# Optimization experiments

Hardware: AMD Instinct MI355X
Metric: run time of the kernel (lower is better)

The kernel has to match this reference:

```python
import jax, jax.numpy as jnp
import numpy as np

SOS = 1
H = 1024
E = 512
V = 32000


def setup_inputs() -> dict:
    key = jax.random.key(0)
    ks = jax.random.split(key, 16)
    B, T_enc, T = 32, 128, 64
    s = 1.0 / np.sqrt(H)
    inp = {
        'encoder_outputs': jax.random.normal(ks[0], (B, T_enc, H), jnp.float32),
        'encoder_hidden': jax.random.normal(ks[1], (1, B, H), jnp.float32),
        'encoder_cell': jax.random.normal(ks[2], (1, B, H), jnp.float32),
        'target_tensor': jax.random.randint(ks[3], (B, T), 0, V),
        'emb_table': jax.random.normal(ks[4], (V, E), jnp.float32) * 0.02,
        'Wa': jax.random.normal(ks[5], (H, H), jnp.float32) * s,
        'Ua': jax.random.normal(ks[6], (H, H), jnp.float32) * s,
        'Va_w': jax.random.normal(ks[7], (1, H), jnp.float32) * s,
        'Va_b': jnp.zeros((1,), jnp.float32),
        'W_ih': jax.random.normal(ks[8], (4 * H, E + H), jnp.float32) * s,
        'W_hh': jax.random.normal(ks[9], (4 * H, H), jnp.float32) * s,
        'b_ih': jnp.zeros((4 * H,), jnp.float32),
        'b_hh': jnp.zeros((4 * H,), jnp.float32),
        'fc_w': jax.random.normal(ks[10], (V, H), jnp.float32) * s,
        'fc_b': jnp.zeros((V,), jnp.float32),
    }
    return inp


def reference(encoder_outputs, encoder_hidden, encoder_cell, target_tensor,
              emb_table, Wa, Ua, Va_w, Va_b, W_ih, W_hh, b_ih, b_hh, fc_w, fc_b):
    B, T = target_tensor.shape
    # padding_idx=0: embedding row 0 is zeros
    emb_table = emb_table.at[0].set(0.0)
    enc_Ua = jnp.einsum('bth,kh->btk', encoder_outputs, Ua)  # precompute Ua(enc)
    # teacher forcing always: inputs are [SOS, target[:, :-1]], shape [T, B]
    tok_seq = jnp.concatenate([jnp.full((B, 1), SOS, target_tensor.dtype),
                               target_tensor[:, :-1]], axis=1).T

    def step(carry, tok):
        h, c = carry  # [B, H]
        emb = emb_table[tok]  # [B, E]
        # Bahdanau attention (query = last-layer hidden)
        q = h @ Wa.T  # [B, H]
        energy = jnp.tanh(q[:, None, :] + enc_Ua)  # [B, T_enc, H]
        scores = jnp.einsum('bth,h->bt', energy, Va_w[0]) + Va_b[0]
        w = jax.nn.softmax(scores, axis=1)
        context = jnp.einsum('bt,bth->bh', w, encoder_outputs)
        x = jnp.concatenate([emb, context], axis=1)  # [B, E+H]
        gates = x @ W_ih.T + b_ih + h @ W_hh.T + b_hh  # [B, 4H], order i,f,g,o
        i, f, g, o = jnp.split(gates, 4, axis=1)
        c = jax.nn.sigmoid(f) * c + jax.nn.sigmoid(i) * jnp.tanh(g)
        h = jax.nn.sigmoid(o) * jnp.tanh(c)
        logp = jax.nn.log_softmax(h @ fc_w.T + fc_b, axis=1)  # [B, V]
        return (h, c), logp

    (h, c), logps = jax.lax.scan(step, (encoder_hidden[0], encoder_cell[0]), tok_seq)
    outputs = jnp.transpose(logps, (1, 0, 2))  # [B, T, V]
    return outputs
```

## Files before the change

kernel.cpp:

```cpp
#include <hip/hip_runtime.h>
#include <math.h>

#define NB 32
#define TE 128
#define NT 64
#define HH 1024
#define EE 512
#define VV 32000
#define GG 4096
#define WQN 5120
#define NBLK 512

typedef __attribute__((ext_vector_type(8))) short bh8;
typedef __attribute__((ext_vector_type(4))) float fx4;
typedef __attribute__((ext_vector_type(4))) unsigned ux4;
typedef __attribute__((ext_vector_type(4))) float fv4;

__device__ __forceinline__ float tanh_fast(float x) {
  float e = __expf(2.f * x);
  return 1.f - 2.f / (e + 1.f);
}
__device__ __forceinline__ float sigf(float x) { return 1.f / (1.f + __expf(-x)); }
__device__ __forceinline__ ushort f2bf(float x) {
  union { float f; unsigned u; } v; v.f = x;
  unsigned r = v.u + 0x7fffu + ((v.u >> 16) & 1u);
  return (ushort)(r >> 16);
}
__device__ __forceinline__ float bf2f(ushort u) {
  return __uint_as_float(((unsigned)u) << 16);
}

__device__ __forceinline__ void st_f32(float* p, float v) {
  __hip_atomic_store(p, v, __ATOMIC_RELAXED, __HIP_MEMORY_SCOPE_AGENT);
}
__device__ __forceinline__ float ld_f32(const float* p) {
  return __hip_atomic_load(p, __ATOMIC_RELAXED, __HIP_MEMORY_SCOPE_AGENT);
}
__device__ __forceinline__ void st_u32(unsigned* p, unsigned v) {
  __hip_atomic_store(p, v, __ATOMIC_RELAXED, __HIP_MEMORY_SCOPE_AGENT);
}
__device__ __forceinline__ unsigned ld_u32(const unsigned* p) {
  return __hip_atomic_load(p, __ATOMIC_RELAXED, __HIP_MEMORY_SCOPE_AGENT);
}

__global__ void k_init(const float* __restrict__ eh, unsigned* __restrict__ h_u32) {
  int i = blockIdx.x * 256 + threadIdx.x;
  float a = eh[i * 2], b = eh[i * 2 + 1];
  h_u32[i] = (unsigned)f2bf(a) | ((unsigned)f2bf(b) << 16);
}

__global__ void k_emb(const int* __restrict__ tgt, const float* __restrict__ etab,
                      ushort* __restrict__ emb_bf) {
  int idx = blockIdx.x * 256 + threadIdx.x;
  int e = idx & (EE - 1);
  int tb = idx >> 9;
  int b = tb & (NB - 1);
  int t = tb >> 5;
  int tok = (t == 0) ? 1 : tgt[b * NT + (t - 1)];
  emb_bf[idx] = (tok == 0) ? (ushort)0 : f2bf(etab[(size_t)tok * EE + e]);
}

__global__ void k_f2b(const float* __restrict__ s, ushort* __restrict__ d, int n4) {
  int i = blockIdx.x * 256 + threadIdx.x;
  if (i >= n4) return;
  float4 v = *(const float4*)(s + (size_t)i * 4);
  *(ushort4*)(d + (size_t)i * 4) = make_ushort4(f2bf(v.x), f2bf(v.y), f2bf(v.z), f2bf(v.w));
}

__global__ void k_f2b_s(const float* __restrict__ s, int ld, int off, int w4,
                        ushort* __restrict__ d, int n) {
  int i = blockIdx.x * 256 + threadIdx.x;
  if (i >= n) return;
  int r = i / w4, c = (i - r * w4) * 4;
  float4 v = *(const float4*)(s + (size_t)r * ld + off + c);
  *(ushort4*)(d + (size_t)r * (w4 * 4) + c) = make_ushort4(f2bf(v.x), f2bf(v.y), f2bf(v.z), f2bf(v.w));
}

__device__ __forceinline__ void stage_pair(const ushort* A, int lda, const ushort* B, int ldb,
    int m0, int n0, int k0, ushort* ldsA, ushort* ldsB, int tid) {
  const int w = tid >> 6;
  const int row = tid >> 2;
  const int kq = (tid & 3) * 8;
  const ushort* ga = A + (size_t)(m0 + row) * lda + k0 + kq;
  const ushort* gb = B + (size_t)(n0 + row) * ldb + k0 + kq;
  ushort* la = ldsA + w * 512;
  ushort* lb = ldsB + w * 512;
  __builtin_amdgcn_global_load_lds((const __attribute__((address_space(1))) void*)ga,
      (__attribute__((address_space(3))) void*)la, 16, 0, 0);
  __builtin_amdgcn_global_load_lds((const __attribute__((address_space(1))) void*)(ga + (size_t)64 * lda),
      (__attribute__((address_space(3))) void*)(la + 2048), 16, 0, 0);
  __builtin_amdgcn_global_load_lds((const __attribute__((address_space(1))) void*)gb,
      (__attribute__((address_space(3))) void*)lb, 16, 0, 0);
  __builtin_amdgcn_global_load_lds((const __attribute__((address_space(1))) void*)(gb + (size_t)64 * ldb),
      (__attribute__((address_space(3))) void*)(lb + 2048), 16, 0, 0);
}

__global__ __launch_bounds__(256) void k_gemm_bf16(
    const ushort* __restrict__ A, int lda,
    const ushort* __restrict__ B, int ldb,
    const float* __restrict__ b1, const float* __restrict__ b2,
    void* __restrict__ Cv, int ldc, int K, int perm, int obf, int swz) {
  __shared__ ushort lds[2][2][4096];
  const int tid = threadIdx.x;
  const int lane = tid & 63, w = tid >> 6;
  int m0, n0;
  if (swz) {
    const int bid = blockIdx.y * gridDim.x + blockIdx.x;
    m0 = (bid & 15) * 128;
    n0 = (bid >> 4) * 128;
  } else {
    m0 = blockIdx.y * 128;
    n0 = blockIdx.x * 128;
  }
  const int wm = (w >> 1) * 64, wn = (w & 1) * 64;
  fx4 acc[4][4] = {};
  stage_pair(A, lda, B, ldb, m0, n0, 0, lds[0][0], lds[0][1], tid);
  __syncthreads();
  const int nk = K >> 5;
  const int ko = (lane >> 4) * 8;
  const int rA = wm + (lane & 15);
  const int rB = wn + (lane & 15);
  for (int ks = 0; ks < nk; ++ks) {
    const int cur = ks & 1;
    if (ks + 1 < nk)
      stage_pair(A, lda, B, ldb, m0, n0, (ks + 1) << 5, lds[cur ^ 1][0], lds[cur ^ 1][1], tid);
    bh8 af[4], bfr[4];
#pragma unroll
    for (int f = 0; f < 4; ++f) {
      af[f]  = *(const bh8*)(&lds[cur][0][(rA + f * 16) * 32 + ko]);
      bfr[f] = *(const bh8*)(&lds[cur][1][(rB + f * 16) * 32 + ko]);
    }
#pragma unroll
    for (int i = 0; i < 4; ++i)
#pragma unroll
      for (int j = 0; j < 4; ++j)
        acc[i][j] = __builtin_amdgcn_mfma_f32_16x16x32_bf16(af[i], bfr[j], acc[i][j], 0, 0, 0);
    __syncthreads();
  }
  float* Cf = (float*)Cv;
  ushort* Cb = (ushort*)Cv;
#pragma unroll
  for (int j = 0; j < 4; ++j) {
    const int col = n0 + wn + j * 16 + (lane & 15);
    const float bv = (b1 ? b1[col] : 0.f) + (b2 ? b2[col] : 0.f);
#pragma unroll
    for (int i = 0; i < 4; ++i) {
      const int mb = m0 + wm + i * 16 + (lane >> 4) * 4;
#pragma unroll
      for (int r = 0; r < 4; ++r) {
        const int m = mb + r;
        const size_t orow = perm ? ((size_t)(m & 31) * 64 + (m >> 5)) : (size_t)m;
        const float v = acc[i][j][r] + bv;
        if (obf) Cb[orow * (size_t)ldc + col] = f2bf(v);
        else     Cf[orow * (size_t)ldc + col] = v;
      }
    }
  }
}

__device__ __forceinline__ void gridbar(unsigned* flags, unsigned* genArr, unsigned epoch) {
  asm volatile("s_waitcnt vmcnt(0)" ::: "memory");
  __syncthreads();
  const int tid = threadIdx.x;
  if (tid == 0) st_u32(flags + blockIdx.x * 32, epoch);
  if (blockIdx.x == 0) {
    while (ld_u32(flags + tid * 32) < epoch) __builtin_amdgcn_s_sleep(1);
    while (ld_u32(flags + (256 + tid) * 32) < epoch) __builtin_amdgcn_s_sleep(1);
    __syncthreads();
    if (tid < 16) st_u32(genArr + tid * 32, epoch);
  } else if (tid == 0) {
    while (ld_u32(genArr + (blockIdx.x & 15) * 32) < epoch) __builtin_amdgcn_s_sleep(1);
  }
  __syncthreads();
}

__global__ __launch_bounds__(256, 1) void k_recur(
    const ushort* __restrict__ Wqh,
    const ushort* __restrict__ encU,
    const ushort* __restrict__ encW,
    const float*  __restrict__ embG,
    const float*  __restrict__ Va,
    const float*  __restrict__ ec,
    float* __restrict__ hW,
    float* __restrict__ sc,
    unsigned* __restrict__ h_u32,
    ushort* __restrict__ hall,
    unsigned* __restrict__ flags, unsigned* __restrict__ genArr) {
  const int bid = blockIdx.x;
  const int tid = threadIdx.x;
  const int lane = tid & 63, w = tid >> 6;
  __shared__ float wlds[4][32][33];
  __shared__ float red[128], wt[TE], gp[4][64];
  __shared__ float cpart[8][4][8][8];
  unsigned epoch = 0;

  const int b3 = bid >> 4, u0 = (bid & 15) * 64;
  float c_r = 0.f;
  if (tid < 64) c_r = ec[b3 * HH + u0 + tid];
  const int bb = bid >> 4, tc = bid & 15;

  for (int t = 0; t < NT; ++t) {
    if (bid < 160) {
      const int n0 = bid * 32;
      const int kb = w * 256;
      const int r15 = lane & 15, ko = (lane >> 4) * 8;
      const char* hbase0 = (const char*)h_u32 + r15 * 2048 + (size_t)(kb + ko) * 2;
      const char* hbase1 = hbase0 + 16 * 2048;
      const ushort* B0 = Wqh + (size_t)(n0 + r15) * HH + kb + ko;
      const ushort* B1 = B0 + 16 * HH;
      fx4 a00 = {}, a01 = {}, a10 = {}, a11 = {};
#pragma unroll
      for (int half = 0; half < 2; ++half) {
        union { ux4 u; bh8 b; } h0[4], h1[4];
        const char* p0 = hbase0 + half * 256;
        const char* p1 = hbase1 + half * 256;
        asm volatile(
          "global_load_dwordx4 %0, %8, off sc0 sc1\n\t"
          "global_load_dwordx4 %1, %8, off offset:64 sc0 sc1\n\t"
          "global_load_dwordx4 %2, %8, off offset:128 sc0 sc1\n\t"
          "global_load_dwordx4 %3, %8, off offset:192 sc0 sc1\n\t"
          "global_load_dwordx4 %4, %9, off sc0 sc1\n\t"
          "global_load_dwordx4 %5, %9, off offset:64 sc0 sc1\n\t"
          "global_load_dwordx4 %6, %9, off offset:128 sc0 sc1\n\t"
          "global_load_dwordx4 %7, %9, off offset:192 sc0 sc1\n\t"
          "s_waitcnt vmcnt(0)"
          : "=&v"(h0[0].u), "=&v"(h0[1].u), "=&v"(h0[2].u), "=&v"(h0[3].u),
            "=&v"(h1[0].u), "=&v"(h1[1].u), "=&v"(h1[2].u), "=&v"(h1[3].u)
          : "v"(p0), "v"(p1));
#pragma unroll
        for (int ks = 0; ks < 4; ++ks) {
          const int k = (half * 4 + ks) * 32;
          bh8 bv0 = *(const bh8*)(B0 + k);
          bh8 bv1 = *(const bh8*)(B1 + k);
          a00 = __builtin_amdgcn_mfma_f32_16x16x32_bf16(h0[ks].b, bv0, a00, 0, 0, 0);
          a01 = __builtin_amdgcn_mfma_f32_16x16x32_bf16(h0[ks].b, bv1, a01, 0, 0, 0);
          a10 = __builtin_amdgcn_mfma_f32_16x16x32_bf16(h1[ks].b, bv0, a10, 0, 0, 0);
          a11 = __builtin_amdgcn_mfma_f32_16x16x32_bf16(h1[ks].b, bv1, a11, 0, 0, 0);
        }
      }
      const int rr = (lane >> 4) * 4;
#pragma unroll
      for (int r = 0; r < 4; ++r) {
        wlds[w][rr + r][r15]           = a00[r];
        wlds[w][rr + r][r15 + 16]      = a01[r];
        wlds[w][16 + rr + r][r15]      = a10[r];
        wlds[w][16 + rr + r][r15 + 16] = a11[r];
      }
      __syncthreads();
      const int row = tid >> 3, c0 = (tid & 7) * 4;
      fv4 s4;
      s4.x = wlds[0][row][c0+0] + wlds[1][row][c0+0] + wlds[2][row][c0+0] + wlds[3][row][c0+0];
      s4.y = wlds[0][row][c0+1] + wlds[1][row][c0+1] + wlds[2][row][c0+1] + wlds[3][row][c0+1];
      s4.z = wlds[0][row][c0+2] + wlds[1][row][c0+2] + wlds[2][row][c0+2] + wlds[3][row][c0+2];
      s4.w = wlds[0][row][c0+3] + wlds[1][row][c0+3] + wlds[2][row][c0+3] + wlds[3][row][c0+3];
      asm volatile("global_store_dwordx4 %0, %1, off sc0 sc1"
                   :: "v"(&hW[row * WQN + n0 + c0]), "v"(s4) : "memory");
    }
    gridbar(flags, genArr, ++epoch);

    {
      union { ux4 u; float f[4]; } q0, q1, q2, q3;
      const float* qp0 = &hW[bb * WQN + lane * 8];
      const float* qp1 = &hW[bb * WQN + 512 + lane * 8];
      asm volatile(
        "global_load_dwordx4 %0, %4, off sc0 sc1\n\t"
        "global_load_dwordx4 %1, %4, off offset:16 sc0 sc1\n\t"
        "global_load_dwordx4 %2, %5, off sc0 sc1\n\t"
        "global_load_dwordx4 %3, %5, off offset:16 sc0 sc1\n\t"
        "s_waitcnt vmcnt(0)"
        : "=&v"(q0.u), "=&v"(q1.u), "=&v"(q2.u), "=&v"(q3.u)
        : "v"(qp0), "v"(qp1));
      float qr[16], vr[16];
#pragma unroll
      for (int j = 0; j < 4; ++j) {
        qr[j] = q0.f[j]; qr[4 + j] = q1.f[j];
        qr[8 + j] = q2.f[j]; qr[12 + j] = q3.f[j];
      }
#pragma unroll
      for (int c = 0; c < 2; ++c) {
        const int h0 = c * 512 + lane * 8;
        float4 va = *(const float4*)(Va + h0);
        float4 vb = *(const float4*)(Va + h0 + 4);
        vr[c*8+0] = va.x; vr[c*8+1] = va.y; vr[c*8+2] = va.z; vr[c*8+3] = va.w;
        vr[c*8+4] = vb.x; vr[c*8+5] = vb.y; vr[c*8+6] = vb.z; vr[c*8+7] = vb.w;
      }
#pragma unroll
      for (int it = 0; it < 2; ++it) {
        const int tt = tc * 8 + w * 2 + it;
        const ushort* ep = encU + (size_t)(bb * TE + tt) * HH;
        float a = 0.f;
#pragma unroll
        for (int c = 0; c < 2; ++c) {
          bh8 e8 = *(const bh8*)(ep + c * 512 + lane * 8);
#pragma unroll
          for (int j = 0; j < 8; ++j)
            a += tanh_fast(qr[c * 8 + j] + bf2f((ushort)e8[j])) * vr[c * 8 + j];
        }
#pragma unroll
        for (int s2 = 32; s2 > 0; s2 >>= 1) a += __shfl_xor(a, s2);
        if (lane == 0) st_f32(&sc[bb * TE + tt], a);
      }
    }
    gridbar(flags, genArr, ++epoch);

    {
      const float sv = (tid < TE) ? ld_f32(&sc[b3 * TE + tid]) : -1e30f;
      if (tid < 128) red[tid] = sv;
      __syncthreads();
      for (int st = 64; st > 0; st >>= 1) {
        if (tid < st) red[tid] = fmaxf(red[tid], red[tid + st]);
        __syncthreads();
      }
      const float mx = red[0];
      __syncthreads();
      const float ev = (tid < TE) ? __expf(sv - mx) : 0.f;
      if (tid < 128) { wt[tid] = ev; red[tid] = ev; }
      __syncthreads();
      for (int st = 64; st > 0; st >>= 1) {
        if (tid < st) red[tid] += red[tid + st];
        __syncthreads();
      }
      const float inv = 1.f / red[0];
      __syncthreads();
      const int oct = tid & 7, g = (tid >> 3) & 3, tq = tid >> 5;
      const ushort* base = encW + (size_t)(b3 * TE + tq * 16) * GG + g * 1024 + u0 + oct * 8;
      float a8[8] = {};
#pragma unroll
      for (int j = 0; j < 16; ++j) {
        bh8 e8 = *(const bh8*)(base + (size_t)j * GG);
        const float wv = wt[tq * 16 + j];
#pragma unroll
        for (int q = 0; q < 8; ++q) a8[q] += wv * bf2f((ushort)e8[q]);
      }
#pragma unroll
      for (int q = 0; q < 8; ++q) cpart[tq][g][oct][q] = a8[q];
      __syncthreads();
      {
        const int c = tid & 63, g2 = tid >> 6;
        float s = 0.f;
#pragma unroll
        for (int q = 0; q < 8; ++q) s += cpart[q][g2][c >> 3][c & 7];
        s *= inv;
        const int cl = g2 * 1024 + u0 + c;
        s += embG[(size_t)(t * NB + b3) * GG + cl];
        float hv;
        asm volatile("global_load_dword %0, %1, off sc0 sc1\n\ts_waitcnt vmcnt(0)"
                     : "=&v"(hv) : "v"(&hW[b3 * WQN + HH + cl]));
        gp[g2][c] = s + hv;
      }
      __syncthreads();
      if (tid < 64) {
        const float gi = gp[0][tid], gf = gp[1][tid];
        const float gg = gp[2][tid], go = gp[3][tid];
        const float cn = sigf(gf) * c_r + sigf(gi) * tanh_fast(gg);
        c_r = cn;
        const float hn = sigf(go) * tanh_fast(cn);
        const float hn_p = __shfl_xor(hn, 1);
        if ((tid & 1) == 0) {
          const ushort hb = f2bf(hn), hb1 = f2bf(hn_p);
          st_u32(&h_u32[b3 * 512 + ((u0 + tid) >> 1)],
                 (unsigned)hb | ((unsigned)hb1 << 16));
          *(ushort2*)(hall + (size_t)t * (NB * HH) + b3 * HH + u0 + tid) = make_ushort2(hb, hb1);
        }
      }
    }
    gridbar(flags, genArr, ++epoch);
  }
}

__global__ __launch_bounds__(256) void k_logsoftmax(float* __restrict__ out) {
  const size_t row = blockIdx.x;
  float* p = out + row * VV;
  __shared__ float sm[256], ss[256];
  const int tid = threadIdx.x;
  float m = -1e30f, s = 0.f;
  for (int i = tid; i < (VV / 4); i += 256) {
    float4 x = *(const float4*)(p + (size_t)i * 4);
    float m4 = fmaxf(fmaxf(x.x, x.y), fmaxf(x.z, x.w));
    float nm = fmaxf(m, m4);
    s = s * __expf(m - nm) + __expf(x.x - nm) + __expf(x.y - nm)
        + __expf(x.z - nm) + __expf(x.w - nm);
    m = nm;
  }
  sm[tid] = m; ss[tid] = s;
  __syncthreads();
  for (int st = 128; st > 0; st >>= 1) {
    if (tid < st) {
      float m2 = fmaxf(sm[tid], sm[tid + st]);
      ss[tid] = ss[tid] * __expf(sm[tid] - m2) + ss[tid + st] * __expf(sm[tid + st] - m2);
      sm[tid] = m2;
    }
    __syncthreads();
  }
  float L = sm[0] + logf(ss[0]);
  __syncthreads();
  for (int i = tid; i < (VV / 4); i += 256) {
    float4 x = *(const float4*)(p + (size_t)i * 4);
    x.x -= L; x.y -= L; x.z -= L; x.w -= L;
    *(float4*)(p + (size_t)i * 4) = x;
  }
}

extern "C" void kernel_launch(void* const* d_in, const int* in_sizes, int n_in,
                              void* d_out, int out_size, void* d_ws, size_t ws_size,
                              hipStream_t stream) {
  const float* enc   = (const float*)d_in[0];
  const float* ehid  = (const float*)d_in[1];
  const float* ecell = (const float*)d_in[2];
  const int*   tgt   = (const int*)d_in[3];
  const float* etab  = (const float*)d_in[4];
  const float* Wa    = (const float*)d_in[5];
  const float* Ua    = (const float*)d_in[6];
  const float* Va_w  = (const float*)d_in[7];
  const float* W_ih  = (const float*)d_in[9];
  const float* W_hh  = (const float*)d_in[10];
  const float* b_ih  = (const float*)d_in[11];
  const float* b_hh  = (const float*)d_in[12];
  const float* fc_w  = (const float*)d_in[13];
  const float* fc_b  = (const float*)d_in[14];
  float* out = (float*)d_out;
  float* ws = (float*)d_ws;

  ushort* encW_bf = (ushort*)ws;
  float*  embG    = ws + 8388608;
  ushort* fcw_bf  = (ushort*)ws;
  ushort* Wqh_bf  = (ushort*)(ws + 16777216);
  ushort* encU_bf = (ushort*)(ws + 19398656);
  ushort* enc_bf  = (ushort*)(ws + 21495808);
  ushort* Wihc_bf = (ushort*)(ws + 23592960);
  ushort* Ua_bf   = (ushort*)(ws + 25690112);
  ushort* emb_bf  = (ushort*)(ws + 26214400);
  ushort* WihE_bf = (ushort*)(ws + 26738688);
  float*  hW      = ws + 21495808;
  float*  sc      = ws + 21659648;
  unsigned* h_u32 = (unsigned*)(ws + 21663744);
  unsigned* flags = (unsigned*)(ws + 27300000);
  unsigned* genArr= (unsigned*)(ws + 27316384);
  ushort* hall_bf = (ushort*)(ws + 27787264);

  k_emb<<<4096, 256, 0, stream>>>(tgt, etab, emb_bf);
  k_f2b<<<4096, 256, 0, stream>>>(enc, enc_bf, 1048576);
  k_f2b<<<1024, 256, 0, stream>>>(Ua, Ua_bf, 262144);
  k_f2b<<<1024, 256, 0, stream>>>(Wa, Wqh_bf, 262144);
  k_f2b<<<4096, 256, 0, stream>>>(W_hh, Wqh_bf + 1024 * HH, 1048576);
  k_f2b_s<<<4096, 256, 0, stream>>>(W_ih, 1536, 512, 256, Wihc_bf, 1048576);
  k_f2b_s<<<2048, 256, 0, stream>>>(W_ih, 1536, 0, 128, WihE_bf, 524288);
  k_gemm_bf16<<<dim3(8, 32), 256, 0, stream>>>(enc_bf, HH, Ua_bf, HH, nullptr, nullptr,
                                               encU_bf, HH, HH, 0, 1, 0);
  k_gemm_bf16<<<dim3(32, 32), 256, 0, stream>>>(enc_bf, HH, Wihc_bf, HH, nullptr, nullptr,
                                                encW_bf, GG, HH, 0, 1, 0);
  k_gemm_bf16<<<dim3(32, 16), 256, 0, stream>>>(emb_bf, EE, WihE_bf, EE, b_ih, b_hh,
                                                embG, GG, EE, 0, 0, 0);
  (void)hipMemsetAsync(flags, 0, (NBLK * 32 + 16 * 32) * sizeof(unsigned), stream);
  k_init<<<64, 256, 0, stream>>>(ehid, h_u32);

  k_recur<<<NBLK, 256, 0, stream>>>(Wqh_bf, encU_bf, encW_bf, embG, Va_w, ecell,
                                    hW, sc, h_u32, hall_bf, flags, genArr);

  k_f2b<<<32000, 256, 0, stream>>>(fc_w, fcw_bf, 8192000);
  k_gemm_bf16<<<dim3(250, 16), 256, 0, stream>>>(hall_bf, HH, fcw_bf, HH, fc_b, nullptr,
                                                 out, VV, HH, 1, 0, 1);
  k_logsoftmax<<<2048, 256, 0, stream>>>(out);
}
```

Baseline: 1.900 ms.

## Split recurrent grid into two independent batch halves with separate grid barriers

The persistent recurrent kernel's 512 blocks are split into two groups of 256, each owning 16 batch rows and using its own flag and generation arrays. Each grid barrier now waits on half as many blocks, and the two groups no longer have to wait on each other. The Wqh projection is computed per half on 16 rows, so each half reads the full Wqh weights every step. That doubles weight traffic in exchange for lower barrier latency and fewer MFMA accumulators per block.

```diff
diff --git a/kernel.cpp b/kernel.cpp
--- a/kernel.cpp
+++ b/kernel.cpp
@@ -158,18 +158,17 @@
   }
 }
 
-__device__ __forceinline__ void gridbar(unsigned* flags, unsigned* genArr, unsigned epoch) {
+__device__ __forceinline__ void gridbar(unsigned* flags, unsigned* genArr, int lb, unsigned epoch) {
   asm volatile("s_waitcnt vmcnt(0)" ::: "memory");
   __syncthreads();
   const int tid = threadIdx.x;
-  if (tid == 0) st_u32(flags + blockIdx.x * 32, epoch);
-  if (blockIdx.x == 0) {
+  if (tid == 0) st_u32(flags + lb * 32, epoch);
+  if (lb == 0) {
     while (ld_u32(flags + tid * 32) < epoch) __builtin_amdgcn_s_sleep(1);
-    while (ld_u32(flags + (256 + tid) * 32) < epoch) __builtin_amdgcn_s_sleep(1);
     __syncthreads();
     if (tid < 16) st_u32(genArr + tid * 32, epoch);
   } else if (tid == 0) {
-    while (ld_u32(genArr + (blockIdx.x & 15) * 32) < epoch) __builtin_amdgcn_s_sleep(1);
+    while (ld_u32(genArr + (lb & 15) * 32) < epoch) __builtin_amdgcn_s_sleep(1);
   }
   __syncthreads();
 }
@@ -187,81 +186,77 @@
     ushort* __restrict__ hall,
     unsigned* __restrict__ flags, unsigned* __restrict__ genArr) {
   const int bid = blockIdx.x;
+  const int half = bid >> 8;
+  const int lb = bid & 255;
+  const int hb0 = half * 16;
+  unsigned* flagsH = flags + half * (256 * 32);
+  unsigned* genH   = genArr + half * (16 * 32);
   const int tid = threadIdx.x;
   const int lane = tid & 63, w = tid >> 6;
-  __shared__ float wlds[4][32][33];
+  __shared__ float wlds[4][16][33];
   __shared__ float red[128], wt[TE], gp[4][64];
   __shared__ float cpart[8][4][8][8];
   unsigned epoch = 0;
 
-  const int b3 = bid >> 4, u0 = (bid & 15) * 64;
+  const int b3 = hb0 + (lb >> 4), u0 = (lb & 15) * 64;
   float c_r = 0.f;
   if (tid < 64) c_r = ec[b3 * HH + u0 + tid];
-  const int bb = bid >> 4, tc = bid & 15;
+  const int bb = b3, tc = lb & 15;
 
   for (int t = 0; t < NT; ++t) {
-    if (bid < 160) {
-      const int n0 = bid * 32;
+    if (lb < 160) {
+      const int n0 = lb * 32;
       const int kb = w * 256;
       const int r15 = lane & 15, ko = (lane >> 4) * 8;
-      const char* hbase0 = (const char*)h_u32 + r15 * 2048 + (size_t)(kb + ko) * 2;
-      const char* hbase1 = hbase0 + 16 * 2048;
+      const char* hbase0 = (const char*)h_u32 + (size_t)(hb0 + r15) * 2048 + (size_t)(kb + ko) * 2;
       const ushort* B0 = Wqh + (size_t)(n0 + r15) * HH + kb + ko;
       const ushort* B1 = B0 + 16 * HH;
-      fx4 a00 = {}, a01 = {}, a10 = {}, a11 = {};
-#pragma unroll
-      for (int half = 0; half < 2; ++half) {
-        union { ux4 u; bh8 b; } h0[4], h1[4];
-        const char* p0 = hbase0 + half * 256;
-        const char* p1 = hbase1 + half * 256;
+      fx4 a00 = {}, a01 = {};
+#pragma unroll
+      for (int hf = 0; hf < 2; ++hf) {
+        union { ux4 u; bh8 b; } h0[4];
+        const char* p0 = hbase0 + hf * 256;
         asm volatile(
-          "global_load_dwordx4 %0, %8, off sc0 sc1\n\t"
-          "global_load_dwordx4 %1, %8, off offset:64 sc0 sc1\n\t"
-          "global_load_dwordx4 %2, %8, off offset:128 sc0 sc1\n\t"
-          "global_load_dwordx4 %3, %8, off offset:192 sc0 sc1\n\t"
-          "global_load_dwordx4 %4, %9, off sc0 sc1\n\t"
-          "global_load_dwordx4 %5, %9, off offset:64 sc0 sc1\n\t"
-          "global_load_dwordx4 %6, %9, off offset:128 sc0 sc1\n\t"
-          "global_load_dwordx4 %7, %9, off offset:192 sc0 sc1\n\t"
+          "global_load_dwordx4 %0, %4, off sc0 sc1\n\t"
+          "global_load_dwordx4 %1, %4, off offset:64 sc0 sc1\n\t"
+          "global_load_dwordx4 %2, %4, off offset:128 sc0 sc1\n\t"
+          "global_load_dwordx4 %3, %4, off offset:192 sc0 sc1\n\t"
           "s_waitcnt vmcnt(0)"
-          : "=&v"(h0[0].u), "=&v"(h0[1].u), "=&v"(h0[2].u), "=&v"(h0[3].u),
-            "=&v"(h1[0].u), "=&v"(h1[1].u), "=&v"(h1[2].u), "=&v"(h1[3].u)
-          : "v"(p0), "v"(p1));
+          : "=&v"(h0[0].u), "=&v"(h0[1].u), "=&v"(h0[2].u), "=&v"(h0[3].u)
+          : "v"(p0));
 #pragma unroll
         for (int ks = 0; ks < 4; ++ks) {
-          const int k = (half * 4 + ks) * 32;
+          const int k = (hf * 4 + ks) * 32;
           bh8 bv0 = *(const bh8*)(B0 + k);
           bh8 bv1 = *(const bh8*)(B1 + k);
           a00 = __builtin_amdgcn_mfma_f32_16x16x32_bf16(h0[ks].b, bv0, a00, 0, 0, 0);
           a01 = __builtin_amdgcn_mfma_f32_16x16x32_bf16(h0[ks].b, bv1, a01, 0, 0, 0);
-          a10 = __builtin_amdgcn_mfma_f32_16x16x32_bf16(h1[ks].b, bv0, a10, 0, 0, 0);
-          a11 = __builtin_amdgcn_mfma_f32_16x16x32_bf16(h1[ks].b, bv1, a11, 0, 0, 0);
         }
       }
       const int rr = (lane >> 4) * 4;
 #pragma unroll
       for (int r = 0; r < 4; ++r) {
-        wlds[w][rr + r][r15]           = a00[r];
-        wlds[w][rr + r][r15 + 16]      = a01[r];
-        wlds[w][16 + rr + r][r15]      = a10[r];
-        wlds[w][16 + rr + r][r15 + 16] = a11[r];
-      }
-      __syncthreads();
-      const int row = tid >> 3, c0 = (tid & 7) * 4;
-      fv4 s4;
-      s4.x = wlds[0][row][c0+0] + wlds[1][row][c0+0] + wlds[2][row][c0+0] + wlds[3][row][c0+0];
-      s4.y = wlds[0][row][c0+1] + wlds[1][row][c0+1] + wlds[2][row][c0+1] + wlds[3][row][c0+1];
-      s4.z = wlds[0][row][c0+2] + wlds[1][row][c0+2] + wlds[2][row][c0+2] + wlds[3][row][c0+2];
-      s4.w = wlds[0][row][c0+3] + wlds[1][row][c0+3] + wlds[2][row][c0+3] + wlds[3][row][c0+3];
-      asm volatile("global_store_dwordx4 %0, %1, off sc0 sc1"
-                   :: "v"(&hW[row * WQN + n0 + c0]), "v"(s4) : "memory");
-    }
-    gridbar(flags, genArr, ++epoch);
+        wlds[w][rr + r][r15]      = a00[r];
+        wlds[w][rr + r][r15 + 16] = a01[r];
+      }
+      __syncthreads();
+      if (tid < 128) {
+        const int row = tid >> 3, c0 = (tid & 7) * 4;
+        fv4 s4;
+        s4.x = wlds[0][row][c0+0] + wlds[1][row][c0+0] + wlds[2][row][c0+0] + wlds[3][row][c0+0];
+        s4.y = wlds[0][row][c0+1] + wlds[1][row][c0+1] + wlds[2][row][c0+1] + wlds[3][row][c0+1];
+        s4.z = wlds[0][row][c0+2] + wlds[1][row][c0+2] + wlds[2][row][c0+2] + wlds[3][row][c0+2];
+        s4.w = wlds[0][row][c0+3] + wlds[1][row][c0+3] + wlds[2][row][c0+3] + wlds[3][row][c0+3];
+        asm volatile("global_store_dwordx4 %0, %1, off sc0 sc1"
+                     :: "v"(&hW[(size_t)(hb0 + row) * WQN + n0 + c0]), "v"(s4) : "memory");
+      }
+    }
+    gridbar(flagsH, genH, lb, ++epoch);
 
     {
       union { ux4 u; float f[4]; } q0, q1, q2, q3;
-      const float* qp0 = &hW[bb * WQN + lane * 8];
-      const float* qp1 = &hW[bb * WQN + 512 + lane * 8];
+      const float* qp0 = &hW[(size_t)bb * WQN + lane * 8];
+      const float* qp1 = &hW[(size_t)bb * WQN + 512 + lane * 8];
       asm volatile(
         "global_load_dwordx4 %0, %4, off sc0 sc1\n\t"
         "global_load_dwordx4 %1, %4, off offset:16 sc0 sc1\n\t"
@@ -301,7 +296,7 @@
         if (lane == 0) st_f32(&sc[bb * TE + tt], a);
       }
     }
-    gridbar(flags, genArr, ++epoch);
+    gridbar(flagsH, genH, lb, ++epoch);
 
     {
       const float sv = (tid < TE) ? ld_f32(&sc[b3 * TE + tid]) : -1e30f;
@@ -345,7 +340,7 @@
         s += embG[(size_t)(t * NB + b3) * GG + cl];
         float hv;
         asm volatile("global_load_dword %0, %1, off sc0 sc1\n\ts_waitcnt vmcnt(0)"
-                     : "=&v"(hv) : "v"(&hW[b3 * WQN + HH + cl]));
+                     : "=&v"(hv) : "v"(&hW[(size_t)b3 * WQN + HH + cl]));
         gp[g2][c] = s + hv;
       }
       __syncthreads();
@@ -364,7 +359,7 @@
         }
       }
     }
-    gridbar(flags, genArr, ++epoch);
+    gridbar(flagsH, genH, lb, ++epoch);
   }
 }
 
@@ -451,7 +446,7 @@
                                                 encW_bf, GG, HH, 0, 1, 0);
   k_gemm_bf16<<<dim3(32, 16), 256, 0, stream>>>(emb_bf, EE, WihE_bf, EE, b_ih, b_hh,
                                                 embG, GG, EE, 0, 0, 0);
-  (void)hipMemsetAsync(flags, 0, (NBLK * 32 + 16 * 32) * sizeof(unsigned), stream);
+  (void)hipMemsetAsync(flags, 0, (512 * 32 + 32 * 32) * sizeof(unsigned), stream);
   k_init<<<64, 256, 0, stream>>>(ehid, h_u32);
 
   k_recur<<<NBLK, 256, 0, stream>>>(Wqh_bf, encU_bf, encW_bf, embG, Va_w, ecell,
```

Measured after the change: 1.815 ms, median of 2. 1.05x faster.
